# Kernel optimization log

Measured on AMD Instinct MI355X. Metric: run time of the kernel, lower is better.

## Reference

```python
import jax, jax.numpy as jnp
import numpy as np

NUM_E = 1024
E_DIM = 64
BETA = 0.5


def setup_inputs() -> dict:
    key = jax.random.key(0)
    k1, k2 = jax.random.split(key)
    z_e = jax.random.normal(k1, (32, E_DIM, 64, 64), dtype=jnp.float32)  # [B, C, H, W]
    codebook = jax.random.uniform(k2, (NUM_E, E_DIM), dtype=jnp.float32,
                                  minval=-1.0 / NUM_E, maxval=1.0 / NUM_E)
    return {"z_e": z_e, "codebook": codebook}


def reference(z_e, codebook):
    B, C, H, W = z_e.shape
    sg = jax.lax.stop_gradient
    z = jnp.transpose(z_e, (0, 2, 3, 1))            # [B, H, W, C]
    zf = z.reshape(-1, C)                           # [N, C]
    # squared L2 distances via ||z||^2 + ||e||^2 - 2 z.e  -> [N, num_e]
    d = (jnp.sum(zf * zf, axis=1, keepdims=True)
         + jnp.sum(codebook * codebook, axis=1)
         - 2.0 * jnp.matmul(zf, codebook.T))
    idx = jnp.argmin(d, axis=1)                     # [N]
    z_q = codebook[idx].reshape(z.shape)            # gather instead of one-hot matmul
    loss = jnp.mean((sg(z_q) - z) ** 2) + BETA * jnp.mean((z_q - sg(z)) ** 2)
    z_q_st = z + sg(z_q - z)                        # straight-through
    # code usage histogram == mean of one-hot encodings
    counts = jnp.zeros((NUM_E,), dtype=z.dtype).at[idx].add(1.0)
    e_mean = counts / idx.shape[0]
    perplexity = jnp.exp(-jnp.sum(e_mean * jnp.log(e_mean + 1e-10)))
    z_q_out = jnp.transpose(z_q_st, (0, 3, 1, 2))   # back to [B, C, H, W]
    return (z_q_out, loss, sg(perplexity), idx.reshape(B, H, W))
```

## Files before the change

### kernel.cpp

```cpp
#include <hip/hip_runtime.h>
#include <math.h>

#define NUM_E   1024
#define ZQ_ELEM 8388608
#define AGRID   256
#define MAXC    7
#define OQCAP   512

typedef short bf16x8 __attribute__((ext_vector_type(8)));
typedef float f32x16 __attribute__((ext_vector_type(16)));

__device__ inline unsigned short rne_bf16(float v) {
    unsigned u = __float_as_uint(v);
    return (unsigned short)((u + 0x7FFFu + ((u >> 16) & 1u)) >> 16);
}

__global__ __launch_bounds__(256) void vq_prep(const float* __restrict__ cb,
                                               float* __restrict__ ee,
                                               unsigned short* __restrict__ ehi)
{
    int j = blockIdx.x * 256 + threadIdx.x;
    const float* r = cb + (size_t)j * 64;
    float v[64];
#pragma unroll
    for (int k = 0; k < 64; ++k) v[k] = r[k];
    float a = 0.f;
#pragma unroll
    for (int k = 0; k < 64; ++k) a = fmaf(v[k], v[k], a);
    ee[j] = a;

    int nt = j >> 5, jc = j & 31;
#pragma unroll
    for (int kt = 0; kt < 4; ++kt)
#pragma unroll
        for (int h = 0; h < 2; ++h) {
            bf16x8 vh;
#pragma unroll
            for (int i = 0; i < 8; ++i)
                vh[i] = (short)rne_bf16(v[kt * 16 + h * 8 + i]);
            *(bf16x8*)(ehi + ((size_t)(nt * 4 + kt) * 64 + h * 32 + jc) * 8) = vh;
        }
}

__device__ inline unsigned long long key_glob(const float* zb, float zz, float eej,
                                              const float* cb, int pl, int j)
{
    const float4* cr = (const float4*)(cb + ((size_t)j << 6));
    float a = 0.f;
#pragma unroll
    for (int qb = 0; qb < 4; ++qb) {
        float4 c0 = cr[qb * 4 + 0];
        float4 c1 = cr[qb * 4 + 1];
        float4 c2 = cr[qb * 4 + 2];
        float4 c3 = cr[qb * 4 + 3];
        float t[16];
#pragma unroll
        for (int i = 0; i < 16; ++i)
            t[i] = zb[(size_t)(qb * 16 + i) * 4096 + pl];
        a = fmaf(t[0],  c0.x, a); a = fmaf(t[1],  c0.y, a);
        a = fmaf(t[2],  c0.z, a); a = fmaf(t[3],  c0.w, a);
        a = fmaf(t[4],  c1.x, a); a = fmaf(t[5],  c1.y, a);
        a = fmaf(t[6],  c1.z, a); a = fmaf(t[7],  c1.w, a);
        a = fmaf(t[8],  c2.x, a); a = fmaf(t[9],  c2.y, a);
        a = fmaf(t[10], c2.z, a); a = fmaf(t[11], c2.w, a);
        a = fmaf(t[12], c3.x, a); a = fmaf(t[13], c3.y, a);
        a = fmaf(t[14], c3.z, a); a = fmaf(t[15], c3.w, a);
    }
    float t1 = zz + eej;
    float d  = fmaf(-2.f, a, t1);
    return ((unsigned long long)__float_as_uint(d) << 32) | (unsigned long long)j;
}

__global__ __launch_bounds__(1024, 4) void vq_argmin(
    const float* __restrict__ z, const float* __restrict__ cb,
    const unsigned short* __restrict__ ehi, const float* __restrict__ ee,
    float* __restrict__ idx_f, int* __restrict__ counts,
    float* __restrict__ zq, double* __restrict__ partials)
{
    __shared__ bf16x8 bB[8192];
    __shared__ float  eeL[1024];
    __shared__ float  zzs[512];
    __shared__ float  wp[512];
    __shared__ unsigned long long best[512];
    __shared__ unsigned short cand[512 * MAXC];
    __shared__ unsigned int ccnt[512];
    __shared__ unsigned int oq[OQCAP];
    __shared__ int ibuf[512];
    __shared__ unsigned int oqcnt, gflow;
    __shared__ double wsum[16];

    const int tid  = threadIdx.x;
    const int g    = blockIdx.x;
    const int lane = tid & 63, wv = tid >> 6;
    const size_t zoff = ((size_t)(g >> 3) << 18) + (size_t)((g & 7) << 9);
    const float* zb = z + zoff;

    eeL[tid] = ee[tid];
    if (tid < 512) { best[tid] = 0xFFFFFFFFFFFFFFFFull; ccnt[tid] = 0; }
    if (tid == 0) { oqcnt = 0; gflow = 0; }
    {
        const uint4* src = (const uint4*)ehi;
        uint4* dst = (uint4*)bB;
#pragma unroll
        for (int i = 0; i < 8; ++i)
            dst[i * 1024 + tid] = src[i * 1024 + tid];
    }

    if (tid < 512) {
        float a = 0.f;
#pragma unroll
        for (int kb = 0; kb < 4; ++kb) {
            float t[16];
#pragma unroll
            for (int i = 0; i < 16; ++i)
                t[i] = zb[(size_t)(kb * 16 + i) * 4096 + tid];
#pragma unroll
            for (int i = 0; i < 16; ++i) a = fmaf(t[i], t[i], a);
        }
        zzs[tid] = a;
    }

    bf16x8 ah[4];
    {
        int h = lane >> 5;
        int pl = wv * 32 + (lane & 31);
        float s1 = 0.f, sd = 0.f;
#pragma unroll
        for (int kt = 0; kt < 4; ++kt) {
            float t[8];
#pragma unroll
            for (int i = 0; i < 8; ++i)
                t[i] = zb[(size_t)(kt * 16 + h * 8 + i) * 4096 + pl];
#pragma unroll
            for (int i = 0; i < 8; ++i) {
                float x = t[i];
                unsigned short hb = rne_bf16(x);
                float hf = __uint_as_float((unsigned)hb << 16);
                ah[kt][i] = (short)hb;
                s1 += fabsf(x);
                sd += fabsf(x - hf);
            }
        }
        s1 += __shfl_xor(s1, 32);
        sd += __shfl_xor(sd, 32);
        if (lane < 32) wp[pl] = 4.f * (s1 * 1.907e-6f + sd * 9.785e-4f) + 1.4e-4f;
    }
    __syncthreads();

    float m[16];
#pragma unroll
    for (int r = 0; r < 16; ++r) m[r] = 3.4e38f;

#define LOADL(B0, B1, B2, B3, EV, ntv) do {                         \
    int _o = (ntv) * 256 + lane;                                    \
    B0 = bB[_o]; B1 = bB[_o + 64]; B2 = bB[_o + 128]; B3 = bB[_o + 192]; \
    EV = eeL[(ntv) * 32 + (lane & 31)];                             \
} while (0)

#define SW1(B0, B1, B2, B3, EV) do {                                \
    f32x16 acc;                                                     \
    _Pragma("unroll")                                               \
    for (int _r = 0; _r < 16; ++_r) acc[_r] = 0.f;                  \
    acc = __builtin_amdgcn_mfma_f32_32x32x16_bf16(ah[0], B0, acc, 0, 0, 0); \
    acc = __builtin_amdgcn_mfma_f32_32x32x16_bf16(ah[1], B1, acc, 0, 0, 0); \
    acc = __builtin_amdgcn_mfma_f32_32x32x16_bf16(ah[2], B2, acc, 0, 0, 0); \
    acc = __builtin_amdgcn_mfma_f32_32x32x16_bf16(ah[3], B3, acc, 0, 0, 0); \
    _Pragma("unroll")                                               \
    for (int _r = 0; _r < 16; ++_r) m[_r] = fminf(m[_r], fmaf(-2.f, acc[_r], EV)); \
} while (0)

    {
        bf16x8 p0, p1, p2, p3, q0, q1, q2, q3;
        float eP, eQ;
        LOADL(p0, p1, p2, p3, eP, 0);
#pragma unroll 1
        for (int nt = 0; nt < 32; nt += 2) {
            LOADL(q0, q1, q2, q3, eQ, nt + 1);
            SW1(p0, p1, p2, p3, eP);
            if (nt + 2 < 32) LOADL(p0, p1, p2, p3, eP, nt + 2);
            SW1(q0, q1, q2, q3, eQ);
        }
    }
#pragma unroll
    for (int r = 0; r < 16; ++r) {
        for (int d2 = 1; d2 <= 16; d2 <<= 1)
            m[r] = fminf(m[r], __shfl_xor(m[r], d2));
        m[r] += wp[wv * 32 + 4 * (lane >> 5) + (r & 3) + 8 * (r >> 2)];
    }

#define ENQ(PL, JJ) do {                                                  \
    unsigned _s = atomicAdd(&ccnt[PL], 1u);                               \
    if (_s < MAXC) cand[(PL) * MAXC + _s] = (unsigned short)(JJ);         \
    else { unsigned _o = atomicAdd(&oqcnt, 1u);                           \
           if (_o < OQCAP) oq[_o] = ((unsigned)(PL) << 16) | (JJ);        \
           else gflow = 1; }                                              \
} while (0)

#define SW2(B0, B1, B2, B3, EV, NTV) do {                           \
    f32x16 acc;                                                     \
    _Pragma("unroll")                                               \
    for (int _r = 0; _r < 16; ++_r) acc[_r] = 0.f;                  \
    acc = __builtin_amdgcn_mfma_f32_32x32x16_bf16(ah[0], B0, acc, 0, 0, 0); \
    acc = __builtin_amdgcn_mfma_f32_32x32x16_bf16(ah[1], B1, acc, 0, 0, 0); \
    acc = __builtin_amdgcn_mfma_f32_32x32x16_bf16(ah[2], B2, acc, 0, 0, 0); \
    acc = __builtin_amdgcn_mfma_f32_32x32x16_bf16(ah[3], B3, acc, 0, 0, 0); \
    unsigned jj = (unsigned)((NTV) * 32 + (lane & 31));             \
    _Pragma("unroll")                                               \
    for (int _r = 0; _r < 16; ++_r) {                               \
        bool hit = fmaf(-2.f, acc[_r], EV) <= m[_r];                \
        if (__any(hit)) {                                           \
            if (hit) {                                              \
                int pl = wv * 32 + 4 * (lane >> 5) + (_r & 3) + 8 * (_r >> 2); \
                ENQ(pl, jj);                                        \
            }                                                       \
        }                                                           \
    }                                                               \
} while (0)

    {
        bf16x8 p0, p1, p2, p3, q0, q1, q2, q3;
        float eP, eQ;
        LOADL(p0, p1, p2, p3, eP, 0);
#pragma unroll 1
        for (int nt = 0; nt < 32; nt += 2) {
            LOADL(q0, q1, q2, q3, eQ, nt + 1);
            SW2(p0, p1, p2, p3, eP, nt);
            if (nt + 2 < 32) LOADL(p0, p1, p2, p3, eP, nt + 2);
            SW2(q0, q1, q2, q3, eQ, nt + 1);
        }
    }
    __syncthreads();

    if (gflow) {
        if (tid < 512) {
            unsigned long long bk = 0xFFFFFFFFFFFFFFFFull;
            for (int j = 0; j < NUM_E; ++j) {
                unsigned long long k2 = key_glob(zb, zzs[tid], eeL[j], cb, tid, j);
                if (k2 < bk) bk = k2;
            }
            best[tid] = bk;
        }
    } else {
        if (tid < 512) {
            int n = (int)ccnt[tid]; if (n > MAXC) n = MAXC;
            unsigned long long bk = 0xFFFFFFFFFFFFFFFFull;
            for (int e = 0; e < n; ++e) {
                int j = (int)cand[tid * MAXC + e];
                unsigned long long k2 = key_glob(zb, zzs[tid], eeL[j], cb, tid, j);
                if (k2 < bk) bk = k2;
            }
            atomicMin(&best[tid], bk);
        }
        int no = (int)oqcnt; if (no > OQCAP) no = OQCAP;
        for (int e = tid; e < no; e += 1024) {
            unsigned u = oq[e];
            int pl = (int)(u >> 16), j = (int)(u & 0xFFFFu);
            atomicMin(&best[pl], key_glob(zb, zzs[pl], eeL[j], cb, pl, j));
        }
    }
    __syncthreads();
    if (tid < 512) {
        int bi = (int)(best[tid] & 0xFFFFFFFFull);
        ibuf[tid] = bi;
        idx_f[(size_t)g * 512 + tid] = (float)bi;
        atomicAdd(&counts[bi], 1);
    }
    __syncthreads();

    {
        int w4 = tid & 127, c8 = (tid >> 7) * 8;
        const float4* zb4 = (const float4*)zb;
        float4* zq4 = (float4*)(zq + zoff);
        size_t b0 = (size_t)ibuf[w4 * 4 + 0] << 6;
        size_t b1 = (size_t)ibuf[w4 * 4 + 1] << 6;
        size_t b2 = (size_t)ibuf[w4 * 4 + 2] << 6;
        size_t b3 = (size_t)ibuf[w4 * 4 + 3] << 6;
        float4 zv[8];
#pragma unroll
        for (int i = 0; i < 8; ++i) zv[i] = zb4[(size_t)(c8 + i) * 1024 + w4];
        double ls = 0.0;
#pragma unroll
        for (int i = 0; i < 8; ++i) {
            int c = c8 + i;
            float q0 = cb[b0 + c], q1 = cb[b1 + c], q2 = cb[b2 + c], q3 = cb[b3 + c];
            float t0 = q0 - zv[i].x, t1 = q1 - zv[i].y, t2 = q2 - zv[i].z, t3 = q3 - zv[i].w;
            zq4[(size_t)c * 1024 + w4] =
                make_float4(zv[i].x + t0, zv[i].y + t1, zv[i].z + t2, zv[i].w + t3);
            ls += (double)t0 * t0 + (double)t1 * t1 + (double)t2 * t2 + (double)t3 * t3;
        }
#pragma unroll
        for (int off = 32; off > 0; off >>= 1) ls += __shfl_down(ls, off);
        if (lane == 0) wsum[wv] = ls;
    }
    __syncthreads();
    if (tid == 0) {
        double s = 0.0;
#pragma unroll
        for (int i = 0; i < 16; ++i) s += wsum[i];
        partials[g] = s;
    }
}

__global__ __launch_bounds__(256) void vq_final(
    const int* __restrict__ counts, const double* __restrict__ partials,
    float* __restrict__ scalars)
{
    __shared__ double sh[256];
    __shared__ double sl[256];
    int t = threadIdx.x;
    double s = 0.0;
    for (int j = t; j < NUM_E; j += 256) {
        float em   = (float)counts[j] * (1.0f / 131072.0f);
        float term = em * logf(em + 1e-10f);
        s += (double)term;
    }
    double l = 0.0;
#pragma unroll
    for (int j = 0; j < AGRID / 256; ++j) l += partials[j * 256 + t];
    sh[t] = s;
    sl[t] = l;
    __syncthreads();
    for (int off = 128; off > 0; off >>= 1) {
        if (t < off) { sh[t] += sh[t + off]; sl[t] += sl[t + off]; }
        __syncthreads();
    }
    if (t == 0) {
        float mm = (float)(sl[0] / 8388608.0);
        scalars[0] = mm + 0.5f * mm;
        scalars[1] = expf(-(float)sh[0]);
    }
}

extern "C" void kernel_launch(void* const* d_in, const int* in_sizes, int n_in,
                              void* d_out, int out_size, void* d_ws, size_t ws_size,
                              hipStream_t stream)
{
    const float* z  = (const float*)d_in[0];
    const float* cb = (const float*)d_in[1];
    float* out     = (float*)d_out;
    float* zq      = out;
    float* scalars = out + ZQ_ELEM;
    float* idx_f   = out + ZQ_ELEM + 2;

    int*            counts   = (int*)d_ws;
    double*         partials = (double*)((char*)d_ws + 4096);
    float*          ee       = (float*)((char*)d_ws + 12288);
    unsigned short* ehi      = (unsigned short*)((char*)d_ws + 16384);

    hipMemsetAsync(d_ws, 0, 4096, stream);
    vq_prep  <<<4,     256, 0, stream>>>(cb, ee, ehi);
    vq_argmin<<<AGRID, 1024, 0, stream>>>(z, cb, ehi, ee, idx_f, counts, zq, partials);
    vq_final <<<1,     256, 0, stream>>>(counts, partials, scalars);
}
```

Baseline: 117.1 us.

## Halve argmin block size and stream second codebook half from global memory

Result: slower. 123.4 us (+5.4%).

```diff
diff --git a/kernel.cpp b/kernel.cpp
--- a/kernel.cpp
+++ b/kernel.cpp
@@ -3,9 +3,9 @@
 
 #define NUM_E   1024
 #define ZQ_ELEM 8388608
-#define AGRID   256
-#define MAXC    7
-#define OQCAP   512
+#define AGRID   512
+#define MAXC    6
+#define OQCAP   256
 
 typedef short bf16x8 __attribute__((ext_vector_type(8)));
 typedef float f32x16 __attribute__((ext_vector_type(16)));
@@ -71,42 +71,44 @@
     return ((unsigned long long)__float_as_uint(d) << 32) | (unsigned long long)j;
 }
 
-__global__ __launch_bounds__(1024, 4) void vq_argmin(
+__global__ __launch_bounds__(512, 4) void vq_argmin(
     const float* __restrict__ z, const float* __restrict__ cb,
     const unsigned short* __restrict__ ehi, const float* __restrict__ ee,
     float* __restrict__ idx_f, int* __restrict__ counts,
     float* __restrict__ zq, double* __restrict__ partials)
 {
-    __shared__ bf16x8 bB[8192];
+    __shared__ bf16x8 bB[4096];
     __shared__ float  eeL[1024];
-    __shared__ float  zzs[512];
-    __shared__ float  wp[512];
-    __shared__ unsigned long long best[512];
-    __shared__ unsigned short cand[512 * MAXC];
-    __shared__ unsigned int ccnt[512];
+    __shared__ float  zzs[256];
+    __shared__ float  wp[256];
+    __shared__ unsigned long long best[256];
+    __shared__ unsigned short cand[256 * MAXC];
+    __shared__ unsigned int ccnt[256];
     __shared__ unsigned int oq[OQCAP];
-    __shared__ int ibuf[512];
+    __shared__ int ibuf[256];
     __shared__ unsigned int oqcnt, gflow;
-    __shared__ double wsum[16];
+    __shared__ double wsum[8];
 
     const int tid  = threadIdx.x;
     const int g    = blockIdx.x;
     const int lane = tid & 63, wv = tid >> 6;
-    const size_t zoff = ((size_t)(g >> 3) << 18) + (size_t)((g & 7) << 9);
+    const size_t zoff = ((size_t)(g >> 4) << 18) + (size_t)((g & 15) << 8);
     const float* zb = z + zoff;
+    const bf16x8* eh8 = (const bf16x8*)ehi;
 
     eeL[tid] = ee[tid];
-    if (tid < 512) { best[tid] = 0xFFFFFFFFFFFFFFFFull; ccnt[tid] = 0; }
+    eeL[tid + 512] = ee[tid + 512];
+    if (tid < 256) { best[tid] = 0xFFFFFFFFFFFFFFFFull; ccnt[tid] = 0; }
     if (tid == 0) { oqcnt = 0; gflow = 0; }
     {
         const uint4* src = (const uint4*)ehi;
         uint4* dst = (uint4*)bB;
 #pragma unroll
         for (int i = 0; i < 8; ++i)
-            dst[i * 1024 + tid] = src[i * 1024 + tid];
-    }
-
-    if (tid < 512) {
+            dst[i * 512 + tid] = src[i * 512 + tid];
+    }
+
+    if (tid < 256) {
         float a = 0.f;
 #pragma unroll
         for (int kb = 0; kb < 4; ++kb) {
@@ -154,6 +156,12 @@
 #define LOADL(B0, B1, B2, B3, EV, ntv) do {                         \
     int _o = (ntv) * 256 + lane;                                    \
     B0 = bB[_o]; B1 = bB[_o + 64]; B2 = bB[_o + 128]; B3 = bB[_o + 192]; \
+    EV = eeL[(ntv) * 32 + (lane & 31)];                             \
+} while (0)
+
+#define LOADG(B0, B1, B2, B3, EV, ntv) do {                         \
+    int _o = (ntv) * 256 + lane;                                    \
+    B0 = eh8[_o]; B1 = eh8[_o + 64]; B2 = eh8[_o + 128]; B3 = eh8[_o + 192]; \
     EV = eeL[(ntv) * 32 + (lane & 31)];                             \
 } while (0)
 
@@ -170,14 +178,22 @@
 } while (0)
 
     {
-        bf16x8 p0, p1, p2, p3, q0, q1, q2, q3;
-        float eP, eQ;
+        bf16x8 p0, p1, p2, p3, q0, q1, q2, q3, r0, r1, r2, r3;
+        float eP, eQ, eR;
+        LOADG(r0, r1, r2, r3, eR, 16);
         LOADL(p0, p1, p2, p3, eP, 0);
 #pragma unroll 1
-        for (int nt = 0; nt < 32; nt += 2) {
+        for (int nt = 0; nt < 16; nt += 2) {
             LOADL(q0, q1, q2, q3, eQ, nt + 1);
             SW1(p0, p1, p2, p3, eP);
-            if (nt + 2 < 32) LOADL(p0, p1, p2, p3, eP, nt + 2);
+            if (nt + 2 < 16) LOADL(p0, p1, p2, p3, eP, nt + 2);
+            SW1(q0, q1, q2, q3, eQ);
+        }
+#pragma unroll 1
+        for (int nt = 16; nt < 32; nt += 2) {
+            LOADG(q0, q1, q2, q3, eQ, nt + 1);
+            SW1(r0, r1, r2, r3, eR);
+            if (nt + 2 < 32) LOADG(r0, r1, r2, r3, eR, nt + 2);
             SW1(q0, q1, q2, q3, eQ);
         }
     }
@@ -218,21 +234,29 @@
 } while (0)
 
     {
-        bf16x8 p0, p1, p2, p3, q0, q1, q2, q3;
-        float eP, eQ;
+        bf16x8 p0, p1, p2, p3, q0, q1, q2, q3, r0, r1, r2, r3;
+        float eP, eQ, eR;
+        LOADG(r0, r1, r2, r3, eR, 16);
         LOADL(p0, p1, p2, p3, eP, 0);
 #pragma unroll 1
-        for (int nt = 0; nt < 32; nt += 2) {
+        for (int nt = 0; nt < 16; nt += 2) {
             LOADL(q0, q1, q2, q3, eQ, nt + 1);
             SW2(p0, p1, p2, p3, eP, nt);
-            if (nt + 2 < 32) LOADL(p0, p1, p2, p3, eP, nt + 2);
+            if (nt + 2 < 16) LOADL(p0, p1, p2, p3, eP, nt + 2);
             SW2(q0, q1, q2, q3, eQ, nt + 1);
         }
+#pragma unroll 1
+        for (int nt = 16; nt < 32; nt += 2) {
+            LOADG(q0, q1, q2, q3, eQ, nt + 1);
+            SW2(r0, r1, r2, r3, eR, nt);
+            if (nt + 2 < 32) LOADG(r0, r1, r2, r3, eR, nt + 2);
+            SW2(q0, q1, q2, q3, eQ, nt + 1);
+        }
     }
     __syncthreads();
 
     if (gflow) {
-        if (tid < 512) {
+        if (tid < 256) {
             unsigned long long bk = 0xFFFFFFFFFFFFFFFFull;
             for (int j = 0; j < NUM_E; ++j) {
                 unsigned long long k2 = key_glob(zb, zzs[tid], eeL[j], cb, tid, j);
@@ -241,7 +265,7 @@
             best[tid] = bk;
         }
     } else {
-        if (tid < 512) {
+        if (tid < 256) {
             int n = (int)ccnt[tid]; if (n > MAXC) n = MAXC;
             unsigned long long bk = 0xFFFFFFFFFFFFFFFFull;
             for (int e = 0; e < n; ++e) {
@@ -252,23 +276,23 @@
             atomicMin(&best[tid], bk);
         }
         int no = (int)oqcnt; if (no > OQCAP) no = OQCAP;
-        for (int e = tid; e < no; e += 1024) {
+        for (int e = tid; e < no; e += 512) {
             unsigned u = oq[e];
             int pl = (int)(u >> 16), j = (int)(u & 0xFFFFu);
             atomicMin(&best[pl], key_glob(zb, zzs[pl], eeL[j], cb, pl, j));
         }
     }
     __syncthreads();
-    if (tid < 512) {
+    if (tid < 256) {
         int bi = (int)(best[tid] & 0xFFFFFFFFull);
         ibuf[tid] = bi;
-        idx_f[(size_t)g * 512 + tid] = (float)bi;
+        idx_f[(size_t)g * 256 + tid] = (float)bi;
         atomicAdd(&counts[bi], 1);
     }
     __syncthreads();
 
     {
-        int w4 = tid & 127, c8 = (tid >> 7) * 8;
+        int w4 = tid & 63, c8 = (tid >> 6) * 8;
         const float4* zb4 = (const float4*)zb;
         float4* zq4 = (float4*)(zq + zoff);
         size_t b0 = (size_t)ibuf[w4 * 4 + 0] << 6;
@@ -296,7 +320,7 @@
     if (tid == 0) {
         double s = 0.0;
 #pragma unroll
-        for (int i = 0; i < 16; ++i) s += wsum[i];
+        for (int i = 0; i < 8; ++i) s += wsum[i];
         partials[g] = s;
     }
 }
@@ -344,11 +368,11 @@
 
     int*            counts   = (int*)d_ws;
     double*         partials = (double*)((char*)d_ws + 4096);
-    float*          ee       = (float*)((char*)d_ws + 12288);
+    float*          ee       = (float*)((char*)d_ws + 8192);
     unsigned short* ehi      = (unsigned short*)((char*)d_ws + 16384);
 
     hipMemsetAsync(d_ws, 0, 4096, stream);
     vq_prep  <<<4,     256, 0, stream>>>(cb, ee, ehi);
-    vq_argmin<<<AGRID, 1024, 0, stream>>>(z, cb, ehi, ee, idx_f, counts, zq, partials);
+    vq_argmin<<<AGRID, 512, 0, stream>>>(z, cb, ehi, ee, idx_f, counts, zq, partials);
     vq_final <<<1,     256, 0, stream>>>(counts, partials, scalars);
 }
```

## Use smaller blocks reading bf16 codebook directly from global instead of LDS

Applied to the files above, without the earlier changes.

Result: slower. 313.7 us (+167.9%).

```diff
diff --git a/kernel.cpp b/kernel.cpp
--- a/kernel.cpp
+++ b/kernel.cpp
@@ -3,9 +3,8 @@
 
 #define NUM_E   1024
 #define ZQ_ELEM 8388608
-#define AGRID   256
-#define MAXC    7
-#define OQCAP   512
+#define AGRID   1024
+#define QCAP    2048
 
 typedef short bf16x8 __attribute__((ext_vector_type(8)));
 typedef float f32x16 __attribute__((ext_vector_type(16)));
@@ -71,42 +70,79 @@
     return ((unsigned long long)__float_as_uint(d) << 32) | (unsigned long long)j;
 }
 
-__global__ __launch_bounds__(1024, 4) void vq_argmin(
+#define LOADB(H, EV, ntv) do {                                      \
+    int _b = (ntv) * 4 * 64 + lane;                                 \
+    _Pragma("unroll")                                               \
+    for (int _k = 0; _k < 4; ++_k) H[_k] = eh8[_b + _k * 64];       \
+    EV = ee[(ntv) * 32 + (lane & 31)];                              \
+} while (0)
+
+#define SW1(H, EV) do {                                             \
+    f32x16 _aA, _aB;                                                \
+    _Pragma("unroll")                                               \
+    for (int _r = 0; _r < 16; ++_r) { _aA[_r] = 0.f; _aB[_r] = 0.f; } \
+    _aA = __builtin_amdgcn_mfma_f32_32x32x16_bf16(ah[0], H[0], _aA, 0, 0, 0); \
+    _aB = __builtin_amdgcn_mfma_f32_32x32x16_bf16(ah[2], H[2], _aB, 0, 0, 0); \
+    _aA = __builtin_amdgcn_mfma_f32_32x32x16_bf16(ah[1], H[1], _aA, 0, 0, 0); \
+    _aB = __builtin_amdgcn_mfma_f32_32x32x16_bf16(ah[3], H[3], _aB, 0, 0, 0); \
+    _Pragma("unroll")                                               \
+    for (int _r = 0; _r < 16; ++_r)                                 \
+        m[_r] = fminf(m[_r], fmaf(-2.f, _aA[_r] + _aB[_r], EV));    \
+} while (0)
+
+#define ENQ(PL, JJ) do {                                            \
+    unsigned _s = atomicAdd(&qcnt, 1u);                             \
+    if (_s < QCAP) queue[_s] = ((unsigned)(PL) << 16) | (JJ);       \
+    else oflow = 1;                                                 \
+} while (0)
+
+#define SW2(H, EV, NTV) do {                                        \
+    f32x16 _aA, _aB;                                                \
+    _Pragma("unroll")                                               \
+    for (int _r = 0; _r < 16; ++_r) { _aA[_r] = 0.f; _aB[_r] = 0.f; } \
+    _aA = __builtin_amdgcn_mfma_f32_32x32x16_bf16(ah[0], H[0], _aA, 0, 0, 0); \
+    _aB = __builtin_amdgcn_mfma_f32_32x32x16_bf16(ah[2], H[2], _aB, 0, 0, 0); \
+    _aA = __builtin_amdgcn_mfma_f32_32x32x16_bf16(ah[1], H[1], _aA, 0, 0, 0); \
+    _aB = __builtin_amdgcn_mfma_f32_32x32x16_bf16(ah[3], H[3], _aB, 0, 0, 0); \
+    unsigned jj = (unsigned)((NTV) * 32 + (lane & 31));             \
+    _Pragma("unroll")                                               \
+    for (int _r = 0; _r < 16; ++_r) {                               \
+        bool hit = fmaf(-2.f, _aA[_r] + _aB[_r], EV) <= m[_r];      \
+        if (__any(hit)) {                                           \
+            if (hit) {                                              \
+                int pl = wv * 32 + 4 * (lane >> 5) + (_r & 3) + 8 * (_r >> 2); \
+                ENQ(pl, jj);                                        \
+            }                                                       \
+        }                                                           \
+    }                                                               \
+} while (0)
+
+__global__ __launch_bounds__(256, 3) void vq_argmin(
     const float* __restrict__ z, const float* __restrict__ cb,
     const unsigned short* __restrict__ ehi, const float* __restrict__ ee,
     float* __restrict__ idx_f, int* __restrict__ counts,
     float* __restrict__ zq, double* __restrict__ partials)
 {
-    __shared__ bf16x8 bB[8192];
-    __shared__ float  eeL[1024];
-    __shared__ float  zzs[512];
-    __shared__ float  wp[512];
-    __shared__ unsigned long long best[512];
-    __shared__ unsigned short cand[512 * MAXC];
-    __shared__ unsigned int ccnt[512];
-    __shared__ unsigned int oq[OQCAP];
-    __shared__ int ibuf[512];
-    __shared__ unsigned int oqcnt, gflow;
-    __shared__ double wsum[16];
+    __shared__ float zzs[128];
+    __shared__ float wp[128];
+    __shared__ unsigned long long best[128];
+    __shared__ unsigned int queue[QCAP];
+    __shared__ unsigned int qcnt;
+    __shared__ unsigned int oflow;
+    __shared__ int ibuf[128];
+    __shared__ double wsum[4];
 
     const int tid  = threadIdx.x;
     const int g    = blockIdx.x;
     const int lane = tid & 63, wv = tid >> 6;
-    const size_t zoff = ((size_t)(g >> 3) << 18) + (size_t)((g & 7) << 9);
+    const size_t zoff = ((size_t)(g >> 5) << 18) + (size_t)((g & 31) << 7);
     const float* zb = z + zoff;
-
-    eeL[tid] = ee[tid];
-    if (tid < 512) { best[tid] = 0xFFFFFFFFFFFFFFFFull; ccnt[tid] = 0; }
-    if (tid == 0) { oqcnt = 0; gflow = 0; }
-    {
-        const uint4* src = (const uint4*)ehi;
-        uint4* dst = (uint4*)bB;
-#pragma unroll
-        for (int i = 0; i < 8; ++i)
-            dst[i * 1024 + tid] = src[i * 1024 + tid];
-    }
-
-    if (tid < 512) {
+    const bf16x8* eh8 = (const bf16x8*)ehi;
+
+    if (tid < 128) best[tid] = 0xFFFFFFFFFFFFFFFFull;
+    if (tid == 0) { qcnt = 0; oflow = 0; }
+
+    if (tid < 128) {
         float a = 0.f;
 #pragma unroll
         for (int kb = 0; kb < 4; ++kb) {
@@ -151,34 +187,20 @@
 #pragma unroll
     for (int r = 0; r < 16; ++r) m[r] = 3.4e38f;
 
-#define LOADL(B0, B1, B2, B3, EV, ntv) do {                         \
-    int _o = (ntv) * 256 + lane;                                    \
-    B0 = bB[_o]; B1 = bB[_o + 64]; B2 = bB[_o + 128]; B3 = bB[_o + 192]; \
-    EV = eeL[(ntv) * 32 + (lane & 31)];                             \
-} while (0)
-
-#define SW1(B0, B1, B2, B3, EV) do {                                \
-    f32x16 acc;                                                     \
-    _Pragma("unroll")                                               \
-    for (int _r = 0; _r < 16; ++_r) acc[_r] = 0.f;                  \
-    acc = __builtin_amdgcn_mfma_f32_32x32x16_bf16(ah[0], B0, acc, 0, 0, 0); \
-    acc = __builtin_amdgcn_mfma_f32_32x32x16_bf16(ah[1], B1, acc, 0, 0, 0); \
-    acc = __builtin_amdgcn_mfma_f32_32x32x16_bf16(ah[2], B2, acc, 0, 0, 0); \
-    acc = __builtin_amdgcn_mfma_f32_32x32x16_bf16(ah[3], B3, acc, 0, 0, 0); \
-    _Pragma("unroll")                                               \
-    for (int _r = 0; _r < 16; ++_r) m[_r] = fminf(m[_r], fmaf(-2.f, acc[_r], EV)); \
-} while (0)
-
     {
-        bf16x8 p0, p1, p2, p3, q0, q1, q2, q3;
-        float eP, eQ;
-        LOADL(p0, p1, p2, p3, eP, 0);
+        bf16x8 b0[4], b1[4], b2[4], b3[4];
+        float e0, e1, e2, e3;
+        LOADB(b0, e0, 0); LOADB(b1, e1, 1); LOADB(b2, e2, 2);
 #pragma unroll 1
-        for (int nt = 0; nt < 32; nt += 2) {
-            LOADL(q0, q1, q2, q3, eQ, nt + 1);
-            SW1(p0, p1, p2, p3, eP);
-            if (nt + 2 < 32) LOADL(p0, p1, p2, p3, eP, nt + 2);
-            SW1(q0, q1, q2, q3, eQ);
+        for (int nt = 0; nt < 32; nt += 4) {
+            LOADB(b3, e3, nt + 3);
+            SW1(b0, e0);
+            if (nt + 4 < 32) LOADB(b0, e0, nt + 4);
+            SW1(b1, e1);
+            if (nt + 5 < 32) LOADB(b1, e1, nt + 5);
+            SW1(b2, e2);
+            if (nt + 6 < 32) LOADB(b2, e2, nt + 6);
+            SW1(b3, e3);
         }
     }
 #pragma unroll
@@ -188,87 +210,52 @@
         m[r] += wp[wv * 32 + 4 * (lane >> 5) + (r & 3) + 8 * (r >> 2)];
     }
 
-#define ENQ(PL, JJ) do {                                                  \
-    unsigned _s = atomicAdd(&ccnt[PL], 1u);                               \
-    if (_s < MAXC) cand[(PL) * MAXC + _s] = (unsigned short)(JJ);         \
-    else { unsigned _o = atomicAdd(&oqcnt, 1u);                           \
-           if (_o < OQCAP) oq[_o] = ((unsigned)(PL) << 16) | (JJ);        \
-           else gflow = 1; }                                              \
-} while (0)
-
-#define SW2(B0, B1, B2, B3, EV, NTV) do {                           \
-    f32x16 acc;                                                     \
-    _Pragma("unroll")                                               \
-    for (int _r = 0; _r < 16; ++_r) acc[_r] = 0.f;                  \
-    acc = __builtin_amdgcn_mfma_f32_32x32x16_bf16(ah[0], B0, acc, 0, 0, 0); \
-    acc = __builtin_amdgcn_mfma_f32_32x32x16_bf16(ah[1], B1, acc, 0, 0, 0); \
-    acc = __builtin_amdgcn_mfma_f32_32x32x16_bf16(ah[2], B2, acc, 0, 0, 0); \
-    acc = __builtin_amdgcn_mfma_f32_32x32x16_bf16(ah[3], B3, acc, 0, 0, 0); \
-    unsigned jj = (unsigned)((NTV) * 32 + (lane & 31));             \
-    _Pragma("unroll")                                               \
-    for (int _r = 0; _r < 16; ++_r) {                               \
-        bool hit = fmaf(-2.f, acc[_r], EV) <= m[_r];                \
-        if (__any(hit)) {                                           \
-            if (hit) {                                              \
-                int pl = wv * 32 + 4 * (lane >> 5) + (_r & 3) + 8 * (_r >> 2); \
-                ENQ(pl, jj);                                        \
-            }                                                       \
-        }                                                           \
-    }                                                               \
-} while (0)
-
     {
-        bf16x8 p0, p1, p2, p3, q0, q1, q2, q3;
-        float eP, eQ;
-        LOADL(p0, p1, p2, p3, eP, 0);
+        bf16x8 b0[4], b1[4], b2[4], b3[4];
+        float e0, e1, e2, e3;
+        LOADB(b0, e0, 0); LOADB(b1, e1, 1); LOADB(b2, e2, 2);
 #pragma unroll 1
-        for (int nt = 0; nt < 32; nt += 2) {
-            LOADL(q0, q1, q2, q3, eQ, nt + 1);
-            SW2(p0, p1, p2, p3, eP, nt);
-            if (nt + 2 < 32) LOADL(p0, p1, p2, p3, eP, nt + 2);
-            SW2(q0, q1, q2, q3, eQ, nt + 1);
-        }
-    }
-    __syncthreads();
-
-    if (gflow) {
-        if (tid < 512) {
+        for (int nt = 0; nt < 32; nt += 4) {
+            LOADB(b3, e3, nt + 3);
+            SW2(b0, e0, nt);
+            if (nt + 4 < 32) LOADB(b0, e0, nt + 4);
+            SW2(b1, e1, nt + 1);
+            if (nt + 5 < 32) LOADB(b1, e1, nt + 5);
+            SW2(b2, e2, nt + 2);
+            if (nt + 6 < 32) LOADB(b2, e2, nt + 6);
+            SW2(b3, e3, nt + 3);
+        }
+    }
+    __syncthreads();
+
+    if (oflow) {
+        if (tid < 128) {
             unsigned long long bk = 0xFFFFFFFFFFFFFFFFull;
             for (int j = 0; j < NUM_E; ++j) {
-                unsigned long long k2 = key_glob(zb, zzs[tid], eeL[j], cb, tid, j);
+                unsigned long long k2 = key_glob(zb, zzs[tid], ee[j], cb, tid, j);
                 if (k2 < bk) bk = k2;
             }
             best[tid] = bk;
         }
     } else {
-        if (tid < 512) {
-            int n = (int)ccnt[tid]; if (n > MAXC) n = MAXC;
-            unsigned long long bk = 0xFFFFFFFFFFFFFFFFull;
-            for (int e = 0; e < n; ++e) {
-                int j = (int)cand[tid * MAXC + e];
-                unsigned long long k2 = key_glob(zb, zzs[tid], eeL[j], cb, tid, j);
-                if (k2 < bk) bk = k2;
-            }
-            atomicMin(&best[tid], bk);
-        }
-        int no = (int)oqcnt; if (no > OQCAP) no = OQCAP;
-        for (int e = tid; e < no; e += 1024) {
-            unsigned u = oq[e];
+        int nq = (int)qcnt;
+        for (int e = tid; e < nq; e += 256) {
+            unsigned u = queue[e];
             int pl = (int)(u >> 16), j = (int)(u & 0xFFFFu);
-            atomicMin(&best[pl], key_glob(zb, zzs[pl], eeL[j], cb, pl, j));
-        }
-    }
-    __syncthreads();
-    if (tid < 512) {
+            atomicMin(&best[pl], key_glob(zb, zzs[pl], ee[j], cb, pl, j));
+        }
+    }
+    __syncthreads();
+    if (tid < 128) {
         int bi = (int)(best[tid] & 0xFFFFFFFFull);
         ibuf[tid] = bi;
-        idx_f[(size_t)g * 512 + tid] = (float)bi;
+        idx_f[(size_t)g * 128 + tid] = (float)bi;
         atomicAdd(&counts[bi], 1);
     }
     __syncthreads();
 
     {
-        int w4 = tid & 127, c8 = (tid >> 7) * 8;
+        int w4 = tid & 31, c8 = (tid >> 5) * 8;
         const float4* zb4 = (const float4*)zb;
         float4* zq4 = (float4*)(zq + zoff);
         size_t b0 = (size_t)ibuf[w4 * 4 + 0] << 6;
@@ -290,15 +277,10 @@
         }
 #pragma unroll
         for (int off = 32; off > 0; off >>= 1) ls += __shfl_down(ls, off);
-        if (lane == 0) wsum[wv] = ls;
-    }
-    __syncthreads();
-    if (tid == 0) {
-        double s = 0.0;
-#pragma unroll
-        for (int i = 0; i < 16; ++i) s += wsum[i];
-        partials[g] = s;
-    }
+        if ((tid & 63) == 0) wsum[tid >> 6] = ls;
+    }
+    __syncthreads();
+    if (tid == 0) partials[g] = wsum[0] + wsum[1] + wsum[2] + wsum[3];
 }
 
 __global__ __launch_bounds__(256) void vq_final(
@@ -349,6 +331,6 @@
 
     hipMemsetAsync(d_ws, 0, 4096, stream);
     vq_prep  <<<4,     256, 0, stream>>>(cb, ee, ehi);
-    vq_argmin<<<AGRID, 1024, 0, stream>>>(z, cb, ehi, ee, idx_f, counts, zq, partials);
+    vq_argmin<<<AGRID, 256, 0, stream>>>(z, cb, ehi, ee, idx_f, counts, zq, partials);
     vq_final <<<1,     256, 0, stream>>>(counts, partials, scalars);
 }
```
